# Performance work log

Hardware: AMD Instinct MI355X
Metric: run time of the kernel (lower is better)

## Reference

```python
import jax, jax.numpy as jnp
import numpy as np

B, D, A, R = 256, 1024, 1024, 8  # batch, feat_dim, ada_dim, rank
I = A  # inter_dim defaults to ada_dim
LN_EPS = 1e-5


def setup_inputs() -> dict:
    key = jax.random.key(0)
    ks = jax.random.split(key, 5)
    return {
        "x": jax.random.normal(ks[0], (B, D), jnp.float32),
        "ada_emb": jax.random.normal(ks[1], (B, A), jnp.float32),
        "base_layer": jax.random.normal(ks[2], (D, D), jnp.float32) * 0.02,
        "ln_gamma": jnp.ones((A,), jnp.float32),
        "ln_beta": jnp.zeros((A,), jnp.float32),
        "W1": jax.random.normal(ks[3], (A, I), jnp.float32) * 0.02,
        "b1": jnp.zeros((I,), jnp.float32),
        "W2": jax.random.normal(ks[4], (I, D * R * 2), jnp.float32) * 0.02,
        "b2": jnp.zeros((D * R * 2,), jnp.float32),
    }


def reference(x, ada_emb, base_layer, ln_gamma, ln_beta, W1, b1, W2, b2):
    Bc, Dc = x.shape
    # norm_cond: LayerNorm over ada_dim
    mu = jnp.mean(ada_emb, axis=-1, keepdims=True)
    var = jnp.var(ada_emb, axis=-1, keepdims=True)
    cond = (ada_emb - mu) * jax.lax.rsqrt(var + LN_EPS) * ln_gamma + ln_beta
    # gen_weight: Linear -> GELU (exact, erf) -> Linear
    h = jax.nn.gelu(cond @ W1 + b1, approximate=False)
    w = h @ W2 + b2                      # [B, 2*D*R]
    x_a, x_b = jnp.split(w, 2, axis=-1)
    x_a = x_a.reshape(Bc, Dc, R)         # [B, D, R]
    x_b = x_b.reshape(Bc, Dc, R)         # [B, D, R]
    # per-sample low-rank weight added to the shared base layer
    layer = base_layer[None, :, :] + jnp.einsum('bdr,bkr->bdk', x_a, x_b)  # [B, D, D]
    out = jnp.einsum('bc,bco->bo', x, layer)
    return x + out  # residual=True
```

## Files before the change

### kernel.cpp

```cpp
#include <hip/hip_runtime.h>
#include <math.h>

#define BB 256
#define DD 1024
#define AA 1024
#define RR 8
#define II 1024
#define NOUT (2*DD*RR)
#define LN_EPS 1e-5f

typedef __attribute__((ext_vector_type(8))) short bf16x8;
typedef __attribute__((ext_vector_type(4))) float f32x4;

__device__ __forceinline__ f32x4 mfma16(bf16x8 a, bf16x8 b, f32x4 c) {
    return __builtin_amdgcn_mfma_f32_16x16x32_bf16(a, b, c, 0, 0, 0);
}

__device__ __forceinline__ unsigned short f2bf(float x) {
    unsigned int u = __float_as_uint(x);
    unsigned int r = (u + 0x7fffu + ((u >> 16) & 1u)) >> 16;
    return (unsigned short)r;
}
__device__ __forceinline__ float bf2f(unsigned short b) {
    return __uint_as_float(((unsigned int)b) << 16);
}
__device__ __forceinline__ void split2(float x, unsigned short& hi, unsigned short& lo) {
    hi = f2bf(x);
    lo = f2bf(x - bf2f(hi));
}

__device__ __forceinline__ float gelu_exact(float v) {
    return 0.5f * v * (1.0f + erff(v * 0.70710678118654752f));
}

__global__ __launch_bounds__(256) void ln_kernel(const float* __restrict__ ada,
                                                 const float* __restrict__ gamma,
                                                 const float* __restrict__ beta,
                                                 float* __restrict__ cond) {
    const int b = blockIdx.x;
    const int tid = threadIdx.x;
    const float4 v = ((const float4*)(ada + (size_t)b * AA))[tid];

    float s  = v.x + v.y + v.z + v.w;
    float ss = v.x * v.x + v.y * v.y + v.z * v.z + v.w * v.w;
    #pragma unroll
    for (int off = 32; off; off >>= 1) {
        s  += __shfl_down(s, off);
        ss += __shfl_down(ss, off);
    }
    __shared__ float red[2][4];
    const int wid = tid >> 6, lane = tid & 63;
    if (lane == 0) { red[0][wid] = s; red[1][wid] = ss; }
    __syncthreads();
    __shared__ float stats[2];
    if (tid == 0) {
        float S  = red[0][0] + red[0][1] + red[0][2] + red[0][3];
        float SS = red[1][0] + red[1][1] + red[1][2] + red[1][3];
        float mu  = S * (1.0f / AA);
        float var = SS * (1.0f / AA) - mu * mu;
        stats[0] = mu;
        stats[1] = rsqrtf(var + LN_EPS);
    }
    __syncthreads();
    const float mu = stats[0], inv = stats[1];
    const float4 g  = ((const float4*)gamma)[tid];
    const float4 be = ((const float4*)beta)[tid];
    float4 o;
    o.x = (v.x - mu) * inv * g.x + be.x;
    o.y = (v.y - mu) * inv * g.y + be.y;
    o.z = (v.z - mu) * inv * g.z + be.z;
    o.w = (v.w - mu) * inv * g.w + be.w;
    ((float4*)(cond + (size_t)b * AA))[tid] = o;
}

__global__ __launch_bounds__(256) void gemm_small(const float* __restrict__ x,
                                                  const float* __restrict__ cond,
                                                  const float* __restrict__ base,
                                                  const float* __restrict__ W1,
                                                  const float* __restrict__ b1,
                                                  float* __restrict__ y,
                                                  unsigned short* __restrict__ h_hi,
                                                  unsigned short* __restrict__ h_lo) {
    __shared__ __align__(16) unsigned short As[2][64][40];
    __shared__ __align__(16) unsigned short Bs[2][64][40];

    const int z = blockIdx.z;
    const float* __restrict__ Asrc = z ? cond : x;
    const float* __restrict__ Bsrc = z ? W1 : base;

    const int tid = threadIdx.x;
    const int bn = blockIdx.x * 64;
    const int bm = blockIdx.y * 64;
    const int wid = tid >> 6, l = tid & 63;
    const int wm = wid >> 1, wn = wid & 1;
    const int lrow = l & 15;
    const int lk = (l >> 4) << 3;

    f32x4 acc[2][2];
    #pragma unroll
    for (int i = 0; i < 2; i++)
        #pragma unroll
        for (int j = 0; j < 2; j++) acc[i][j] = (f32x4)0.0f;

    const int an = tid & 63, akq = (tid >> 6) << 2;

    for (int k0 = 0; k0 < 1024; k0 += 32) {
        #pragma unroll
        for (int i = 0; i < 2; i++) {
            int slot = tid + i * 256;
            int row = slot >> 3, kq = (slot & 7) << 2;
            float4 v = *(const float4*)&Asrc[(size_t)(bm + row) * 1024 + k0 + kq];
            ushort4 H, L;
            split2(v.x, H.x, L.x); split2(v.y, H.y, L.y);
            split2(v.z, H.z, L.z); split2(v.w, H.w, L.w);
            *(ushort4*)&As[0][row][kq] = H;
            *(ushort4*)&As[1][row][kq] = L;
        }
        #pragma unroll
        for (int h = 0; h < 32; h += 16) {
            float v[4];
            #pragma unroll
            for (int i = 0; i < 4; i++)
                v[i] = Bsrc[(size_t)(k0 + akq + h + i) * 1024 + bn + an];
            ushort4 H, L;
            split2(v[0], H.x, L.x); split2(v[1], H.y, L.y);
            split2(v[2], H.z, L.z); split2(v[3], H.w, L.w);
            *(ushort4*)&Bs[0][an][akq + h] = H;
            *(ushort4*)&Bs[1][an][akq + h] = L;
        }
        __syncthreads();

        bf16x8 a[2][2], bf[2][2];
        #pragma unroll
        for (int pl = 0; pl < 2; pl++) {
            #pragma unroll
            for (int mi = 0; mi < 2; mi++)
                a[pl][mi] = *(const bf16x8*)&As[pl][wm * 32 + mi * 16 + lrow][lk];
            #pragma unroll
            for (int ni = 0; ni < 2; ni++)
                bf[pl][ni] = *(const bf16x8*)&Bs[pl][wn * 32 + ni * 16 + lrow][lk];
        }
        #pragma unroll
        for (int mi = 0; mi < 2; mi++)
            #pragma unroll
            for (int ni = 0; ni < 2; ni++) {
                acc[mi][ni] = mfma16(a[0][mi], bf[0][ni], acc[mi][ni]);
                acc[mi][ni] = mfma16(a[0][mi], bf[1][ni], acc[mi][ni]);
                acc[mi][ni] = mfma16(a[1][mi], bf[0][ni], acc[mi][ni]);
            }
        __syncthreads();
    }

    #pragma unroll
    for (int mi = 0; mi < 2; mi++) {
        #pragma unroll
        for (int ni = 0; ni < 2; ni++) {
            const int row0 = bm + wm * 32 + mi * 16 + (l >> 4) * 4;
            const int col  = bn + wn * 32 + ni * 16 + lrow;
            #pragma unroll
            for (int j = 0; j < 4; j++) {
                float v = acc[mi][ni][j];
                if (z == 0) {
                    y[(size_t)(row0 + j) * 1024 + col] = v;
                } else {
                    float g = gelu_exact(v + b1[col]);
                    unsigned short hi, lo;
                    split2(g, hi, lo);
                    h_hi[(size_t)(row0 + j) * 1024 + col] = hi;
                    h_lo[(size_t)(row0 + j) * 1024 + col] = lo;
                }
            }
        }
    }
}

__global__ __launch_bounds__(512) void gemm_big(const unsigned short* __restrict__ Ahi,
                                                const unsigned short* __restrict__ Alo,
                                                const float* __restrict__ Bm,
                                                const float* __restrict__ bias,
                                                float* __restrict__ Cm) {
    __shared__ __align__(16) unsigned short As[2][256][40];
    __shared__ __align__(16) unsigned short Bs[2][64][40];

    const int tid = threadIdx.x;
    const int bn = blockIdx.x * 64;
    const int wid = tid >> 6, l = tid & 63;
    const int lrow = l & 15;
    const int lk = (l >> 4) << 3;

    f32x4 acc[2][4];
    #pragma unroll
    for (int i = 0; i < 2; i++)
        #pragma unroll
        for (int j = 0; j < 4; j++) acc[i][j] = (f32x4)0.0f;

    const int sn = tid & 63, skq = (tid >> 6) << 2;

    for (int k0 = 0; k0 < 1024; k0 += 32) {
        #pragma unroll
        for (int i = 0; i < 4; i++) {
            int slot = tid + i * 512;
            int row = slot >> 3, kq = (slot & 7) << 2;
            *(ushort4*)&As[0][row][kq] = *(const ushort4*)&Ahi[(size_t)row * II + k0 + kq];
            *(ushort4*)&As[1][row][kq] = *(const ushort4*)&Alo[(size_t)row * II + k0 + kq];
        }
        {
            float v[4];
            #pragma unroll
            for (int i = 0; i < 4; i++)
                v[i] = Bm[(size_t)(k0 + skq + i) * NOUT + bn + sn];
            ushort4 H, L;
            split2(v[0], H.x, L.x); split2(v[1], H.y, L.y);
            split2(v[2], H.z, L.z); split2(v[3], H.w, L.w);
            *(ushort4*)&Bs[0][sn][skq] = H;
            *(ushort4*)&Bs[1][sn][skq] = L;
        }
        __syncthreads();

        bf16x8 a[2][2], bf[2][4];
        #pragma unroll
        for (int pl = 0; pl < 2; pl++) {
            #pragma unroll
            for (int mi = 0; mi < 2; mi++)
                a[pl][mi] = *(const bf16x8*)&As[pl][wid * 32 + mi * 16 + lrow][lk];
            #pragma unroll
            for (int ni = 0; ni < 4; ni++)
                bf[pl][ni] = *(const bf16x8*)&Bs[pl][ni * 16 + lrow][lk];
        }
        #pragma unroll
        for (int mi = 0; mi < 2; mi++)
            #pragma unroll
            for (int ni = 0; ni < 4; ni++) {
                acc[mi][ni] = mfma16(a[0][mi], bf[0][ni], acc[mi][ni]);
                acc[mi][ni] = mfma16(a[0][mi], bf[1][ni], acc[mi][ni]);
                acc[mi][ni] = mfma16(a[1][mi], bf[0][ni], acc[mi][ni]);
            }
        __syncthreads();
    }

    #pragma unroll
    for (int mi = 0; mi < 2; mi++) {
        #pragma unroll
        for (int ni = 0; ni < 4; ni++) {
            const int row0 = wid * 32 + mi * 16 + (l >> 4) * 4;
            const int col  = bn + ni * 16 + lrow;
            const float bv = bias[col];
            #pragma unroll
            for (int j = 0; j < 4; j++)
                Cm[(size_t)(row0 + j) * NOUT + col] = acc[mi][ni][j] + bv;
        }
    }
}

__global__ __launch_bounds__(256) void t_kernel(const float* __restrict__ x,
                                                const float* __restrict__ w,
                                                float* __restrict__ tmat) {
    const int b = blockIdx.x;
    const int tid = threadIdx.x;
    const float* wa = w + (size_t)b * NOUT;
    const float4 xv = ((const float4*)(x + (size_t)b * DD))[tid];
    const float xs[4] = {xv.x, xv.y, xv.z, xv.w};

    float acc[RR] = {};
    #pragma unroll
    for (int i = 0; i < 4; i++) {
        const int c = tid * 4 + i;
        const float4 w0 = *(const float4*)&wa[c * RR];
        const float4 w1 = *(const float4*)&wa[c * RR + 4];
        acc[0] = fmaf(xs[i], w0.x, acc[0]);
        acc[1] = fmaf(xs[i], w0.y, acc[1]);
        acc[2] = fmaf(xs[i], w0.z, acc[2]);
        acc[3] = fmaf(xs[i], w0.w, acc[3]);
        acc[4] = fmaf(xs[i], w1.x, acc[4]);
        acc[5] = fmaf(xs[i], w1.y, acc[5]);
        acc[6] = fmaf(xs[i], w1.z, acc[6]);
        acc[7] = fmaf(xs[i], w1.w, acc[7]);
    }
    __shared__ float red[4][RR];
    const int wid = tid >> 6, lane = tid & 63;
    #pragma unroll
    for (int r = 0; r < RR; r++) {
        float v = acc[r];
        #pragma unroll
        for (int off = 32; off; off >>= 1) v += __shfl_down(v, off);
        if (lane == 0) red[wid][r] = v;
    }
    __syncthreads();
    if (tid < RR) {
        tmat[b * RR + tid] = red[0][tid] + red[1][tid] + red[2][tid] + red[3][tid];
    }
}

__global__ __launch_bounds__(256) void final_kernel(const float* __restrict__ x,
                                                    const float* __restrict__ y,
                                                    const float* __restrict__ w,
                                                    const float* __restrict__ tmat,
                                                    float* __restrict__ out) {
    const int b = blockIdx.x;
    const int tid = threadIdx.x;
    float tr[RR];
    #pragma unroll
    for (int r = 0; r < RR; r++) tr[r] = tmat[b * RR + r];

    const float* wb = w + (size_t)b * NOUT + DD * RR;
    const int o0 = tid * 4;
    const float4 xv = *(const float4*)&x[(size_t)b * DD + o0];
    const float4 yv = *(const float4*)&y[(size_t)b * DD + o0];

    float vals[4];
    #pragma unroll
    for (int i = 0; i < 4; i++) {
        const float4 w0 = *(const float4*)&wb[(o0 + i) * RR];
        const float4 w1 = *(const float4*)&wb[(o0 + i) * RR + 4];
        vals[i] = tr[0] * w0.x + tr[1] * w0.y + tr[2] * w0.z + tr[3] * w0.w
                + tr[4] * w1.x + tr[5] * w1.y + tr[6] * w1.z + tr[7] * w1.w;
    }
    float4 o;
    o.x = xv.x + yv.x + vals[0];
    o.y = xv.y + yv.y + vals[1];
    o.z = xv.z + yv.z + vals[2];
    o.w = xv.w + yv.w + vals[3];
    *(float4*)&out[(size_t)b * DD + o0] = o;
}

extern "C" void kernel_launch(void* const* d_in, const int* in_sizes, int n_in,
                              void* d_out, int out_size, void* d_ws, size_t ws_size,
                              hipStream_t stream) {
    const float* x     = (const float*)d_in[0];
    const float* ada   = (const float*)d_in[1];
    const float* base  = (const float*)d_in[2];
    const float* gamma = (const float*)d_in[3];
    const float* beta  = (const float*)d_in[4];
    const float* W1    = (const float*)d_in[5];
    const float* b1    = (const float*)d_in[6];
    const float* W2    = (const float*)d_in[7];
    const float* b2    = (const float*)d_in[8];
    float* out = (float*)d_out;

    char* wsb = (char*)d_ws;
    float* w    = (float*)(wsb);
    float* y    = (float*)(wsb + 16777216);
    float* cond = (float*)(wsb + 17825792);
    unsigned short* h_hi = (unsigned short*)(wsb + 18874368);
    unsigned short* h_lo = (unsigned short*)(wsb + 19398656);
    float* tmat = (float*)(wsb + 19922944);

    ln_kernel<<<BB, 256, 0, stream>>>(ada, gamma, beta, cond);

    gemm_small<<<dim3(DD / 64, BB / 64, 2), 256, 0, stream>>>(
        x, cond, base, W1, b1, y, h_hi, h_lo);

    gemm_big<<<dim3(NOUT / 64, 1), 512, 0, stream>>>(h_hi, h_lo, W2, b2, w);

    t_kernel<<<BB, 256, 0, stream>>>(x, w, tmat);

    final_kernel<<<BB, 256, 0, stream>>>(x, y, w, tmat, out);
}
```

Before: 203.3 us.

## Double-buffer GEMM tiles with direct global-to-LDS loads and pre-split activations

Both GEMMs now double-buffer their shared-memory tiles. The next K-slice of the weight operand is loaded into registers, and the bf16 hi/lo activation chunks are copied straight into LDS with global_load_lds, both while MFMAs run on the current buffer. The hi/lo split of x and of the LayerNorm output moves into the LN kernel, and LDS is reorganised into a 16-row chunked layout that matches the 16-byte direct loads. The base-layer product is written into the output buffer instead of a separate workspace. This aims to hide global-load latency and remove one barrier per iteration, at the cost of more LDS and registers.

```diff
diff --git a/kernel.cpp b/kernel.cpp
--- a/kernel.cpp
+++ b/kernel.cpp
@@ -12,6 +12,13 @@
 typedef __attribute__((ext_vector_type(8))) short bf16x8;
 typedef __attribute__((ext_vector_type(4))) float f32x4;
 
+typedef const __attribute__((address_space(1))) unsigned int gu32_t;
+typedef __attribute__((address_space(3))) unsigned int lu32_t;
+
+__device__ __forceinline__ void glds16(void* lds, const void* g) {
+    __builtin_amdgcn_global_load_lds((gu32_t*)g, (lu32_t*)lds, 16, 0, 0);
+}
+
 __device__ __forceinline__ f32x4 mfma16(bf16x8 a, bf16x8 b, f32x4 c) {
     return __builtin_amdgcn_mfma_f32_16x16x32_bf16(a, b, c, 0, 0, 0);
 }
@@ -33,10 +40,14 @@
     return 0.5f * v * (1.0f + erff(v * 0.70710678118654752f));
 }
 
-__global__ __launch_bounds__(256) void ln_kernel(const float* __restrict__ ada,
-                                                 const float* __restrict__ gamma,
-                                                 const float* __restrict__ beta,
-                                                 float* __restrict__ cond) {
+__global__ __launch_bounds__(256) void ln_split_kernel(const float* __restrict__ ada,
+                                                       const float* __restrict__ xp,
+                                                       const float* __restrict__ gamma,
+                                                       const float* __restrict__ beta,
+                                                       unsigned short* __restrict__ c_hi,
+                                                       unsigned short* __restrict__ c_lo,
+                                                       unsigned short* __restrict__ x_hi,
+                                                       unsigned short* __restrict__ x_lo) {
     const int b = blockIdx.x;
     const int tid = threadIdx.x;
     const float4 v = ((const float4*)(ada + (size_t)b * AA))[tid];
@@ -65,27 +76,40 @@
     const float mu = stats[0], inv = stats[1];
     const float4 g  = ((const float4*)gamma)[tid];
     const float4 be = ((const float4*)beta)[tid];
-    float4 o;
-    o.x = (v.x - mu) * inv * g.x + be.x;
-    o.y = (v.y - mu) * inv * g.y + be.y;
-    o.z = (v.z - mu) * inv * g.z + be.z;
-    o.w = (v.w - mu) * inv * g.w + be.w;
-    ((float4*)(cond + (size_t)b * AA))[tid] = o;
-}
-
-__global__ __launch_bounds__(256) void gemm_small(const float* __restrict__ x,
-                                                  const float* __restrict__ cond,
+    float o[4];
+    o[0] = (v.x - mu) * inv * g.x + be.x;
+    o[1] = (v.y - mu) * inv * g.y + be.y;
+    o[2] = (v.z - mu) * inv * g.z + be.z;
+    o[3] = (v.w - mu) * inv * g.w + be.w;
+    ushort4 H, L;
+    split2(o[0], H.x, L.x); split2(o[1], H.y, L.y);
+    split2(o[2], H.z, L.z); split2(o[3], H.w, L.w);
+    ((ushort4*)(c_hi + (size_t)b * AA))[tid] = H;
+    ((ushort4*)(c_lo + (size_t)b * AA))[tid] = L;
+
+    const float4 xv = ((const float4*)(xp + (size_t)b * DD))[tid];
+    split2(xv.x, H.x, L.x); split2(xv.y, H.y, L.y);
+    split2(xv.z, H.z, L.z); split2(xv.w, H.w, L.w);
+    ((ushort4*)(x_hi + (size_t)b * DD))[tid] = H;
+    ((ushort4*)(x_lo + (size_t)b * DD))[tid] = L;
+}
+
+__global__ __launch_bounds__(256) void gemm_small(const unsigned short* __restrict__ x_hi,
+                                                  const unsigned short* __restrict__ x_lo,
+                                                  const unsigned short* __restrict__ c_hi,
+                                                  const unsigned short* __restrict__ c_lo,
                                                   const float* __restrict__ base,
                                                   const float* __restrict__ W1,
                                                   const float* __restrict__ b1,
-                                                  float* __restrict__ y,
+                                                  float* __restrict__ outy,
                                                   unsigned short* __restrict__ h_hi,
                                                   unsigned short* __restrict__ h_lo) {
-    __shared__ __align__(16) unsigned short As[2][64][40];
-    __shared__ __align__(16) unsigned short Bs[2][64][40];
+    __shared__ __align__(16) unsigned short As[2][4096];
+    __shared__ __align__(16) unsigned short Bs[2][4096];
 
     const int z = blockIdx.z;
-    const float* __restrict__ Asrc = z ? cond : x;
+    const unsigned short* __restrict__ Ahi = z ? c_hi : x_hi;
+    const unsigned short* __restrict__ Alo = z ? c_lo : x_lo;
     const float* __restrict__ Bsrc = z ? W1 : base;
 
     const int tid = threadIdx.x;
@@ -93,8 +117,8 @@
     const int bm = blockIdx.y * 64;
     const int wid = tid >> 6, l = tid & 63;
     const int wm = wid >> 1, wn = wid & 1;
-    const int lrow = l & 15;
-    const int lk = (l >> 4) << 3;
+    const int kg = l >> 4;
+    const int lr16 = (l & 15) * 16;
 
     f32x4 acc[2][2];
     #pragma unroll
@@ -102,68 +126,104 @@
         #pragma unroll
         for (int j = 0; j < 2; j++) acc[i][j] = (f32x4)0.0f;
 
-    const int an = tid & 63, akq = (tid >> 6) << 2;
-
-    for (int k0 = 0; k0 < 1024; k0 += 32) {
-        #pragma unroll
-        for (int i = 0; i < 2; i++) {
-            int slot = tid + i * 256;
-            int row = slot >> 3, kq = (slot & 7) << 2;
-            float4 v = *(const float4*)&Asrc[(size_t)(bm + row) * 1024 + k0 + kq];
-            ushort4 H, L;
-            split2(v.x, H.x, L.x); split2(v.y, H.y, L.y);
-            split2(v.z, H.z, L.z); split2(v.w, H.w, L.w);
-            *(ushort4*)&As[0][row][kq] = H;
-            *(ushort4*)&As[1][row][kq] = L;
-        }
-        #pragma unroll
-        for (int h = 0; h < 32; h += 16) {
-            float v[4];
-            #pragma unroll
-            for (int i = 0; i < 4; i++)
-                v[i] = Bsrc[(size_t)(k0 + akq + h + i) * 1024 + bn + an];
-            ushort4 H, L;
-            split2(v[0], H.x, L.x); split2(v[1], H.y, L.y);
-            split2(v[2], H.z, L.z); split2(v[3], H.w, L.w);
-            *(ushort4*)&Bs[0][an][akq + h] = H;
-            *(ushort4*)&Bs[1][an][akq + h] = L;
+    const int sn = l;
+    const int skq = (tid >> 6) << 2;
+    const int s_nblk = sn >> 4, s_lr16 = (sn & 15) * 16;
+
+    float v[8];
+    #pragma unroll
+    for (int h = 0; h < 2; h++)
+        #pragma unroll
+        for (int i = 0; i < 4; i++)
+            v[h * 4 + i] = Bsrc[(size_t)(skq + 16 * h + i) * 1024 + bn + sn];
+    #pragma unroll
+    for (int i = 0; i < 2; i++) {
+        const int ch = wid * 2 + i;
+        const unsigned short* src = (ch < 4) ? Ahi : Alo;
+        const int row = bm + (ch & 3) * 16 + (l & 15);
+        glds16((char*)As[0] + ch * 1024, src + (size_t)row * 1024 + kg * 8);
+    }
+    #pragma unroll
+    for (int h = 0; h < 2; h++) {
+        ushort4 H, L;
+        split2(v[h*4+0], H.x, L.x); split2(v[h*4+1], H.y, L.y);
+        split2(v[h*4+2], H.z, L.z); split2(v[h*4+3], H.w, L.w);
+        const int kbyte = (skq + 16 * h) * 2;
+        const int kch = kbyte >> 4, low = kbyte & 15;
+        *(ushort4*)((char*)Bs[0] + ((0 * 4 + s_nblk) * 4 + kch) * 256 + s_lr16 + low) = H;
+        *(ushort4*)((char*)Bs[0] + ((1 * 4 + s_nblk) * 4 + kch) * 256 + s_lr16 + low) = L;
+    }
+    __syncthreads();
+
+    int cur = 0;
+    for (int t = 0; t < 32; ++t) {
+        const bool pf = (t < 31);
+        const int k0n = (t + 1) * 32;
+        if (pf) {
+            #pragma unroll
+            for (int h = 0; h < 2; h++)
+                #pragma unroll
+                for (int i = 0; i < 4; i++)
+                    v[h * 4 + i] = Bsrc[(size_t)(k0n + skq + 16 * h + i) * 1024 + bn + sn];
+            #pragma unroll
+            for (int i = 0; i < 2; i++) {
+                const int ch = wid * 2 + i;
+                const unsigned short* src = (ch < 4) ? Ahi : Alo;
+                const int row = bm + (ch & 3) * 16 + (l & 15);
+                glds16((char*)As[cur ^ 1] + ch * 1024, src + (size_t)row * 1024 + k0n + kg * 8);
+            }
+        }
+        {
+            bf16x8 a[2][2], bb[2][2];
+            #pragma unroll
+            for (int pl = 0; pl < 2; pl++) {
+                #pragma unroll
+                for (int mi = 0; mi < 2; mi++)
+                    a[pl][mi] = *(const bf16x8*)((const char*)As[cur] +
+                        ((pl * 4 + wm * 2 + mi) * 4 + kg) * 256 + lr16);
+                #pragma unroll
+                for (int ni = 0; ni < 2; ni++)
+                    bb[pl][ni] = *(const bf16x8*)((const char*)Bs[cur] +
+                        ((pl * 4 + wn * 2 + ni) * 4 + kg) * 256 + lr16);
+            }
+            #pragma unroll
+            for (int mi = 0; mi < 2; mi++)
+                #pragma unroll
+                for (int ni = 0; ni < 2; ni++) {
+                    acc[mi][ni] = mfma16(a[0][mi], bb[0][ni], acc[mi][ni]);
+                    acc[mi][ni] = mfma16(a[0][mi], bb[1][ni], acc[mi][ni]);
+                    acc[mi][ni] = mfma16(a[1][mi], bb[0][ni], acc[mi][ni]);
+                }
+        }
+        if (pf) {
+            #pragma unroll
+            for (int h = 0; h < 2; h++) {
+                ushort4 H, L;
+                split2(v[h*4+0], H.x, L.x); split2(v[h*4+1], H.y, L.y);
+                split2(v[h*4+2], H.z, L.z); split2(v[h*4+3], H.w, L.w);
+                const int kbyte = (skq + 16 * h) * 2;
+                const int kch = kbyte >> 4, low = kbyte & 15;
+                *(ushort4*)((char*)Bs[cur ^ 1] + ((0 * 4 + s_nblk) * 4 + kch) * 256 + s_lr16 + low) = H;
+                *(ushort4*)((char*)Bs[cur ^ 1] + ((1 * 4 + s_nblk) * 4 + kch) * 256 + s_lr16 + low) = L;
+            }
         }
         __syncthreads();
-
-        bf16x8 a[2][2], bf[2][2];
-        #pragma unroll
-        for (int pl = 0; pl < 2; pl++) {
-            #pragma unroll
-            for (int mi = 0; mi < 2; mi++)
-                a[pl][mi] = *(const bf16x8*)&As[pl][wm * 32 + mi * 16 + lrow][lk];
-            #pragma unroll
-            for (int ni = 0; ni < 2; ni++)
-                bf[pl][ni] = *(const bf16x8*)&Bs[pl][wn * 32 + ni * 16 + lrow][lk];
-        }
-        #pragma unroll
-        for (int mi = 0; mi < 2; mi++)
-            #pragma unroll
-            for (int ni = 0; ni < 2; ni++) {
-                acc[mi][ni] = mfma16(a[0][mi], bf[0][ni], acc[mi][ni]);
-                acc[mi][ni] = mfma16(a[0][mi], bf[1][ni], acc[mi][ni]);
-                acc[mi][ni] = mfma16(a[1][mi], bf[0][ni], acc[mi][ni]);
-            }
-        __syncthreads();
+        cur ^= 1;
     }
 
     #pragma unroll
     for (int mi = 0; mi < 2; mi++) {
         #pragma unroll
         for (int ni = 0; ni < 2; ni++) {
-            const int row0 = bm + wm * 32 + mi * 16 + (l >> 4) * 4;
-            const int col  = bn + wn * 32 + ni * 16 + lrow;
+            const int row0 = bm + wm * 32 + mi * 16 + kg * 4;
+            const int col  = bn + wn * 32 + ni * 16 + (l & 15);
             #pragma unroll
             for (int j = 0; j < 4; j++) {
-                float v = acc[mi][ni][j];
+                float val = acc[mi][ni][j];
                 if (z == 0) {
-                    y[(size_t)(row0 + j) * 1024 + col] = v;
+                    outy[(size_t)(row0 + j) * 1024 + col] = val;
                 } else {
-                    float g = gelu_exact(v + b1[col]);
+                    float g = gelu_exact(val + b1[col]);
                     unsigned short hi, lo;
                     split2(g, hi, lo);
                     h_hi[(size_t)(row0 + j) * 1024 + col] = hi;
@@ -179,14 +239,14 @@
                                                 const float* __restrict__ Bm,
                                                 const float* __restrict__ bias,
                                                 float* __restrict__ Cm) {
-    __shared__ __align__(16) unsigned short As[2][256][40];
-    __shared__ __align__(16) unsigned short Bs[2][64][40];
+    __shared__ __align__(16) unsigned short As[2][16384];
+    __shared__ __align__(16) unsigned short Bs[2][4096];
 
     const int tid = threadIdx.x;
-    const int bn = blockIdx.x * 64;
+    const int bn  = blockIdx.x * 64;
     const int wid = tid >> 6, l = tid & 63;
-    const int lrow = l & 15;
-    const int lk = (l >> 4) << 3;
+    const int kg = l >> 4;
+    const int lr16 = (l & 15) * 16;
 
     f32x4 acc[2][4];
     #pragma unroll
@@ -194,56 +254,87 @@
         #pragma unroll
         for (int j = 0; j < 4; j++) acc[i][j] = (f32x4)0.0f;
 
-    const int sn = tid & 63, skq = (tid >> 6) << 2;
-
-    for (int k0 = 0; k0 < 1024; k0 += 32) {
-        #pragma unroll
-        for (int i = 0; i < 4; i++) {
-            int slot = tid + i * 512;
-            int row = slot >> 3, kq = (slot & 7) << 2;
-            *(ushort4*)&As[0][row][kq] = *(const ushort4*)&Ahi[(size_t)row * II + k0 + kq];
-            *(ushort4*)&As[1][row][kq] = *(const ushort4*)&Alo[(size_t)row * II + k0 + kq];
+    const int sn = l;
+    const int skq = wid * 4;
+    const int s_nblk = sn >> 4, s_lr16 = (sn & 15) * 16;
+    const int s_kbyte = skq * 2;
+    const int s_kch = s_kbyte >> 4, s_low = s_kbyte & 15;
+
+    float v[4];
+    #pragma unroll
+    for (int i = 0; i < 4; i++)
+        v[i] = Bm[(size_t)(skq + i) * NOUT + bn + sn];
+    #pragma unroll
+    for (int i = 0; i < 4; i++) {
+        const int ch = wid * 4 + i;
+        const unsigned short* src = (ch < 16) ? Ahi : Alo;
+        const int row = (ch & 15) * 16 + (l & 15);
+        glds16((char*)As[0] + ch * 1024, src + (size_t)row * II + kg * 8);
+    }
+    {
+        ushort4 H, L;
+        split2(v[0], H.x, L.x); split2(v[1], H.y, L.y);
+        split2(v[2], H.z, L.z); split2(v[3], H.w, L.w);
+        *(ushort4*)((char*)Bs[0] + ((0 * 4 + s_nblk) * 4 + s_kch) * 256 + s_lr16 + s_low) = H;
+        *(ushort4*)((char*)Bs[0] + ((1 * 4 + s_nblk) * 4 + s_kch) * 256 + s_lr16 + s_low) = L;
+    }
+    __syncthreads();
+
+    int cur = 0;
+    for (int t = 0; t < 32; ++t) {
+        const bool pf = (t < 31);
+        const int k0n = (t + 1) * 32;
+        if (pf) {
+            #pragma unroll
+            for (int i = 0; i < 4; i++)
+                v[i] = Bm[(size_t)(k0n + skq + i) * NOUT + bn + sn];
+            #pragma unroll
+            for (int i = 0; i < 4; i++) {
+                const int ch = wid * 4 + i;
+                const unsigned short* src = (ch < 16) ? Ahi : Alo;
+                const int row = (ch & 15) * 16 + (l & 15);
+                glds16((char*)As[cur ^ 1] + ch * 1024, src + (size_t)row * II + k0n + kg * 8);
+            }
         }
         {
-            float v[4];
-            #pragma unroll
-            for (int i = 0; i < 4; i++)
-                v[i] = Bm[(size_t)(k0 + skq + i) * NOUT + bn + sn];
+            bf16x8 a[2][2], bb[2][4];
+            #pragma unroll
+            for (int pl = 0; pl < 2; pl++) {
+                #pragma unroll
+                for (int mi = 0; mi < 2; mi++)
+                    a[pl][mi] = *(const bf16x8*)((const char*)As[cur] +
+                        ((pl * 16 + wid * 2 + mi) * 4 + kg) * 256 + lr16);
+                #pragma unroll
+                for (int ni = 0; ni < 4; ni++)
+                    bb[pl][ni] = *(const bf16x8*)((const char*)Bs[cur] +
+                        ((pl * 4 + ni) * 4 + kg) * 256 + lr16);
+            }
+            #pragma unroll
+            for (int mi = 0; mi < 2; mi++)
+                #pragma unroll
+                for (int ni = 0; ni < 4; ni++) {
+                    acc[mi][ni] = mfma16(a[0][mi], bb[0][ni], acc[mi][ni]);
+                    acc[mi][ni] = mfma16(a[0][mi], bb[1][ni], acc[mi][ni]);
+                    acc[mi][ni] = mfma16(a[1][mi], bb[0][ni], acc[mi][ni]);
+                }
+        }
+        if (pf) {
             ushort4 H, L;
             split2(v[0], H.x, L.x); split2(v[1], H.y, L.y);
             split2(v[2], H.z, L.z); split2(v[3], H.w, L.w);
-            *(ushort4*)&Bs[0][sn][skq] = H;
-            *(ushort4*)&Bs[1][sn][skq] = L;
+            *(ushort4*)((char*)Bs[cur ^ 1] + ((0 * 4 + s_nblk) * 4 + s_kch) * 256 + s_lr16 + s_low) = H;
+            *(ushort4*)((char*)Bs[cur ^ 1] + ((1 * 4 + s_nblk) * 4 + s_kch) * 256 + s_lr16 + s_low) = L;
         }
         __syncthreads();
-
-        bf16x8 a[2][2], bf[2][4];
-        #pragma unroll
-        for (int pl = 0; pl < 2; pl++) {
-            #pragma unroll
-            for (int mi = 0; mi < 2; mi++)
-                a[pl][mi] = *(const bf16x8*)&As[pl][wid * 32 + mi * 16 + lrow][lk];
-            #pragma unroll
-            for (int ni = 0; ni < 4; ni++)
-                bf[pl][ni] = *(const bf16x8*)&Bs[pl][ni * 16 + lrow][lk];
-        }
-        #pragma unroll
-        for (int mi = 0; mi < 2; mi++)
-            #pragma unroll
-            for (int ni = 0; ni < 4; ni++) {
-                acc[mi][ni] = mfma16(a[0][mi], bf[0][ni], acc[mi][ni]);
-                acc[mi][ni] = mfma16(a[0][mi], bf[1][ni], acc[mi][ni]);
-                acc[mi][ni] = mfma16(a[1][mi], bf[0][ni], acc[mi][ni]);
-            }
-        __syncthreads();
+        cur ^= 1;
     }
 
     #pragma unroll
     for (int mi = 0; mi < 2; mi++) {
         #pragma unroll
         for (int ni = 0; ni < 4; ni++) {
-            const int row0 = wid * 32 + mi * 16 + (l >> 4) * 4;
-            const int col  = bn + ni * 16 + lrow;
+            const int row0 = wid * 32 + mi * 16 + kg * 4;
+            const int col  = bn + ni * 16 + (l & 15);
             const float bv = bias[col];
             #pragma unroll
             for (int j = 0; j < 4; j++)
@@ -280,10 +371,10 @@
     const int wid = tid >> 6, lane = tid & 63;
     #pragma unroll
     for (int r = 0; r < RR; r++) {
-        float v = acc[r];
-        #pragma unroll
-        for (int off = 32; off; off >>= 1) v += __shfl_down(v, off);
-        if (lane == 0) red[wid][r] = v;
+        float vv = acc[r];
+        #pragma unroll
+        for (int off = 32; off; off >>= 1) vv += __shfl_down(vv, off);
+        if (lane == 0) red[wid][r] = vv;
     }
     __syncthreads();
     if (tid < RR) {
@@ -292,7 +383,6 @@
 }
 
 __global__ __launch_bounds__(256) void final_kernel(const float* __restrict__ x,
-                                                    const float* __restrict__ y,
                                                     const float* __restrict__ w,
                                                     const float* __restrict__ tmat,
                                                     float* __restrict__ out) {
@@ -305,7 +395,7 @@
     const float* wb = w + (size_t)b * NOUT + DD * RR;
     const int o0 = tid * 4;
     const float4 xv = *(const float4*)&x[(size_t)b * DD + o0];
-    const float4 yv = *(const float4*)&y[(size_t)b * DD + o0];
+    const float4 yv = *(const float4*)&out[(size_t)b * DD + o0];
 
     float vals[4];
     #pragma unroll
@@ -338,21 +428,23 @@
     float* out = (float*)d_out;
 
     char* wsb = (char*)d_ws;
-    float* w    = (float*)(wsb);
-    float* y    = (float*)(wsb + 16777216);
-    float* cond = (float*)(wsb + 17825792);
-    unsigned short* h_hi = (unsigned short*)(wsb + 18874368);
-    unsigned short* h_lo = (unsigned short*)(wsb + 19398656);
+    float* w = (float*)(wsb);
+    unsigned short* h_hi = (unsigned short*)(wsb + 16777216);
+    unsigned short* h_lo = (unsigned short*)(wsb + 17301504);
+    unsigned short* x_hi = (unsigned short*)(wsb + 17825792);
+    unsigned short* x_lo = (unsigned short*)(wsb + 18350080);
+    unsigned short* c_hi = (unsigned short*)(wsb + 18874368);
+    unsigned short* c_lo = (unsigned short*)(wsb + 19398656);
     float* tmat = (float*)(wsb + 19922944);
 
-    ln_kernel<<<BB, 256, 0, stream>>>(ada, gamma, beta, cond);
+    ln_split_kernel<<<BB, 256, 0, stream>>>(ada, x, gamma, beta, c_hi, c_lo, x_hi, x_lo);
 
     gemm_small<<<dim3(DD / 64, BB / 64, 2), 256, 0, stream>>>(
-        x, cond, base, W1, b1, y, h_hi, h_lo);
+        x_hi, x_lo, c_hi, c_lo, base, W1, b1, out, h_hi, h_lo);
 
     gemm_big<<<dim3(NOUT / 64, 1), 512, 0, stream>>>(h_hi, h_lo, W2, b2, w);
 
     t_kernel<<<BB, 256, 0, stream>>>(x, w, tmat);
 
-    final_kernel<<<BB, 256, 0, stream>>>(x, y, w, tmat, out);
-}
+    final_kernel<<<BB, 256, 0, stream>>>(x, w, tmat, out);
+}
```

Measured after the change: 208.1 us. 1.02x slower.
